# Performance work log

Hardware: AMD Instinct MI355X
Metric: run time of the kernel (lower is better)

Reference implementation:

```python
import jax, jax.numpy as jnp
import numpy as np

B, S, D = 4, 4096, 64   # batch, seq_len, input_size
H, HD = 4, 16           # num_heads, head_dim


def setup_inputs() -> dict:
    key = jax.random.key(0)
    ks = jax.random.split(key, 9)
    sd = 1.0 / np.sqrt(D)          # torch Linear default uniform(-1/sqrt(fan_in), ...)
    so = 1.0 / np.sqrt(H * HD)
    u = lambda k, shape, s: jax.random.uniform(k, shape, jnp.float32, -s, s)
    return {
        "x": jax.random.normal(ks[0], (B, S, D), jnp.float32),
        "Wq": u(ks[1], (H, D, HD), sd), "bq": u(ks[2], (H, HD), sd),
        "Wk": u(ks[3], (H, D, HD), sd), "bk": u(ks[4], (H, HD), sd),
        "Wv": u(ks[5], (H, D, HD), sd), "bv": u(ks[6], (H, HD), sd),
        "Wo": u(ks[7], (H * HD, D), so), "bo": u(ks[8], (D,), so),
    }


def reference(x, Wq, bq, Wk, bk, Wv, bv, Wo, bo):
    # Batched per-head projections (fuses the original per-head Linear loop)
    q = jnp.einsum('bsd,hde->bhse', x, Wq) + bq[None, :, None, :]
    k = jnp.einsum('bsd,hde->bhse', x, Wk) + bk[None, :, None, :]
    v = jnp.einsum('bsd,hde->bhse', x, Wv) + bv[None, :, None, :]
    # scores: [B, H, S(query), S(key)]
    scores = jnp.einsum('bhse,bhte->bhst', q, k) / np.sqrt(HD).astype(np.float32)
    # FAITHFUL quirk: torch Softmax(dim=1) on [B,S,S] normalizes over the QUERY axis
    w = jax.nn.softmax(scores, axis=2)
    attended = jnp.einsum('bhst,bhte->bhse', w, v)          # [B,H,S,HD]
    concat = attended.transpose(0, 2, 1, 3).reshape(B, S, H * HD)
    out = concat @ Wo + bo                                   # [B,S,D]
    # FAITHFUL quirk: final softmax over the sequence axis (dim=1)
    return jax.nn.softmax(out, axis=1)
```

## Files before the change

### kernel.cpp

```cpp
#include <hip/hip_runtime.h>
#include <hip/hip_bf16.h>


#define BB 4
#define SS 4096
#define DD 64
#define HH 4
#define HDD 16

typedef unsigned int u32;
typedef unsigned short u16;
typedef __attribute__((ext_vector_type(8))) short bfrag;
typedef __attribute__((ext_vector_type(4))) float floatx4;
typedef __attribute__((ext_vector_type(16))) float floatx16;
typedef __attribute__((ext_vector_type(2))) u32 u32x2;
typedef __attribute__((ext_vector_type(4))) u32 u32x4;

#define LOG2E 1.4426950408889634074f
#define QSCALE (LOG2E * 0.25f)

__device__ __forceinline__ float fexp2(float x) {
#if __has_builtin(__builtin_amdgcn_exp2f)
  return __builtin_amdgcn_exp2f(x);
#else
  float r; asm("v_exp_f32 %0, %1" : "=v"(r) : "v"(x)); return r;
#endif
}
__device__ __forceinline__ float frcp(float x) {
#if __has_builtin(__builtin_amdgcn_rcpf)
  return __builtin_amdgcn_rcpf(x);
#else
  float r; asm("v_rcp_f32 %0, %1" : "=v"(r) : "v"(x)); return r;
#endif
}

__device__ __forceinline__ u16 f2bf(float f) {
  u32 u = __builtin_bit_cast(u32, f);
  return (u16)((u + 0x7FFFu + ((u >> 16) & 1u)) >> 16);
}
__device__ __forceinline__ u32 pack_bf(float lo, float hi) {
#if __has_builtin(__builtin_amdgcn_perm)
  return __builtin_amdgcn_perm(__builtin_bit_cast(u32, hi),
                               __builtin_bit_cast(u32, lo), 0x07060302u);
#else
  u32 a = __builtin_bit_cast(u32, lo);
  u32 b = __builtin_bit_cast(u32, hi);
  return (a >> 16) | (b & 0xFFFF0000u);
#endif
}

__global__ __launch_bounds__(256) void k_proj(
    const float* __restrict__ x,
    const float* __restrict__ Wq, const float* __restrict__ bq,
    const float* __restrict__ Wk, const float* __restrict__ bk,
    const float* __restrict__ Wv, const float* __restrict__ bv,
    u16* __restrict__ qb, u16* __restrict__ kb, float* __restrict__ vf)
{
  __shared__ float xs[16 * 64];
  const int tid = threadIdx.x;
  const int blk = blockIdx.x;
  const int b   = blk >> 8;
  const int s0  = (blk & 255) << 4;
  ((float4*)xs)[tid] = ((const float4*)(x + ((size_t)b * SS + s0) * DD))[tid];
  __syncthreads();

  const int col = tid & 63, h = col >> 4, e = col & 15;
  const int rg  = tid >> 6;
  float aq[4] = {0,0,0,0}, ak[4] = {0,0,0,0}, av[4] = {0,0,0,0};
  const int wofs = h * (DD * HDD) + e;
#pragma unroll 4
  for (int d = 0; d < DD; ++d) {
    float wq = Wq[wofs + d * HDD];
    float wk = Wk[wofs + d * HDD];
    float wv = Wv[wofs + d * HDD];
    const float* xr = xs + (rg * 4) * 64 + d;
#pragma unroll
    for (int r = 0; r < 4; ++r) {
      float xv = xr[r * 64];
      aq[r] += xv * wq; ak[r] += xv * wk; av[r] += xv * wv;
    }
  }
  const float bqv = bq[col], bkv = bk[col], bvv = bv[col];
  size_t base = ((size_t)(b * HH + h) * SS + (s0 + rg * 4)) * HDD + e;
#pragma unroll
  for (int r = 0; r < 4; ++r) {
    qb[base + r * HDD] = f2bf((aq[r] + bqv) * QSCALE);
    kb[base + r * HDD] = f2bf(ak[r] + bkv);
    vf[base + r * HDD] = av[r] + bvv;
  }
}

__global__ __launch_bounds__(256, 8) void k_colsum(
    const u16* __restrict__ qb, const u16* __restrict__ kb,
    float* __restrict__ csp)
{
  const int tid = threadIdx.x;
  const int lane = tid & 63, w = tid >> 6;
  const int l31 = lane & 31, hl = lane >> 5;
  const int bh = blockIdx.z, chunk = blockIdx.y;
  const int t0 = blockIdx.x * 128 + w * 32;
  const size_t base = (size_t)bh * (SS * HDD);

  const bfrag kf = *(const bfrag*)(kb + base + (size_t)(t0 + l31) * HDD + hl * 8);
  const u16* qp = qb + base + (size_t)l31 * HDD + hl * 8;
  const floatx16 z16 = {0.f};
  float c = 0.f;
  const int s0 = chunk * 1024;
#pragma unroll 2
  for (int s = s0; s < s0 + 1024; s += 32) {
    bfrag qfr = *(const bfrag*)(qp + (size_t)s * HDD);
    floatx16 d = __builtin_amdgcn_mfma_f32_32x32x16_bf16(qfr, kf, z16, 0, 0, 0);
#pragma unroll
    for (int i = 0; i < 16; ++i) c += fexp2(d[i]);
  }
  c += __shfl_xor(c, 32, 64);
  if (hl == 0)
    csp[((size_t)bh * 4 + chunk) * SS + t0 + l31] = c;
}

__global__ __launch_bounds__(256, 6) void k_attn(
    const u16* __restrict__ qb, const u16* __restrict__ kb,
    const float* __restrict__ vf, const float* __restrict__ csp,
    float* __restrict__ attp)
{
  __shared__ __align__(16) u16 vls[16 * 520];
  __shared__ float rcs[512];
  const int tid  = threadIdx.x;
  const int lane = tid & 63, w = tid >> 6;
  const int l31 = lane & 31, hl = lane >> 5;
  const int bh = blockIdx.z, b = bh >> 2, h = bh & 3;
  const int tq = blockIdx.y;
  const int s0 = blockIdx.x * 128 + w * 32;
  const size_t base = (size_t)bh * (SS * HDD);

  const bfrag qf = *(const bfrag*)(qb + base + (size_t)(s0 + l31) * HDD + hl * 8);
  const u16* kp = kb + base + (size_t)l31 * HDD + hl * 8;
  const u16* vrow = vls + (l31 & 15) * 520 + hl * 16;
  const floatx16 z16 = {0.f};
  floatx16 acc = {0.f};

  for (int th = 0; th < 2; ++th) {
    const int tb = tq * 1024 + th * 512;
    __syncthreads();
    {
      const float* cp0 = csp + (size_t)bh * 4 * SS + tb;
#pragma unroll
      for (int i = 0; i < 2; ++i) {
        int j = i * 256 + tid;
        rcs[j] = frcp(cp0[j] + cp0[j + SS] + cp0[j + 2 * SS] + cp0[j + 3 * SS]);
      }
    }
    __syncthreads();
    {
      const float4* vsrc = (const float4*)(vf + base + (size_t)tb * HDD);
#pragma unroll
      for (int kk = 0; kk < 8; ++kk) {
        int c = kk * 256 + tid;
        int tl = c >> 2, g = c & 3;
        float4 vv = vsrc[c];
        float rc = rcs[tl];
        int i5 = tl >> 5, t5 = tl & 31;
        int sub = ((t5 >> 2) & 1) * 16 + ((t5 >> 3) << 2) + (t5 & 3);
        u16* wp = vls + i5 * 32 + sub;
        wp[(4 * g + 0) * 520] = f2bf(vv.x * rc);
        wp[(4 * g + 1) * 520] = f2bf(vv.y * rc);
        wp[(4 * g + 2) * 520] = f2bf(vv.z * rc);
        wp[(4 * g + 3) * 520] = f2bf(vv.w * rc);
      }
    }
    __syncthreads();

#pragma unroll 2
    for (int it = 0; it < 16; ++it) {
      bfrag kf = *(const bfrag*)(kp + (size_t)(tb + it * 32) * HDD);
      floatx16 d = __builtin_amdgcn_mfma_f32_32x32x16_bf16(kf, qf, z16, 0, 0, 0);
      u32 wr[8];
#pragma unroll
      for (int p = 0; p < 8; ++p)
        wr[p] = pack_bf(fexp2(d[2 * p]), fexp2(d[2 * p + 1]));
      const u16* va = vrow + it * 32;
      u32x4 af0 = *(const u32x4*)(va);
      u32x4 af1 = *(const u32x4*)(va + 8);
      u32x4 ef0 = {wr[0], wr[1], wr[2], wr[3]};
      u32x4 ef1 = {wr[4], wr[5], wr[6], wr[7]};
      acc = __builtin_amdgcn_mfma_f32_32x32x16_bf16(
          __builtin_bit_cast(bfrag, af0), __builtin_bit_cast(bfrag, ef0), acc, 0, 0, 0);
      acc = __builtin_amdgcn_mfma_f32_32x32x16_bf16(
          __builtin_bit_cast(bfrag, af1), __builtin_bit_cast(bfrag, ef1), acc, 0, 0, 0);
    }
  }

  float* ao = attp + (((size_t)tq * BB + b) * SS + s0 + l31) * (HH * HDD)
            + h * HDD + 4 * hl;
  float4 lo4 = {acc[0], acc[1], acc[2], acc[3]};
  float4 hi4 = {acc[4], acc[5], acc[6], acc[7]};
  *(float4*)ao       = lo4;
  *(float4*)(ao + 8) = hi4;
}

__global__ __launch_bounds__(256) void k_oproj(
    const float* __restrict__ att, const float* __restrict__ Wo,
    const float* __restrict__ bo, float* __restrict__ outp,
    float* __restrict__ part)
{
  __shared__ float wols[64 * 64];
  __shared__ float red[4][64];
  const int tid = threadIdx.x;
  const int blk = blockIdx.x;
  const int b = blk >> 9, s0 = (blk & 511) << 3;
#pragma unroll
  for (int i = 0; i < 4; ++i)
    ((float4*)wols)[tid + 256 * i] = ((const float4*)Wo)[tid + 256 * i];
  __syncthreads();

  const int d = tid & 63, sg = tid >> 6;
  const float bov = bo[d];
  const size_t so = (size_t)BB * SS * 16;
  float es = 0.f;
#pragma unroll
  for (int r = 0; r < 2; ++r) {
    int s = s0 + sg * 2 + r;
    const floatx4* row = (const floatx4*)(att + ((size_t)b * SS + s) * 64);
    float acc = bov;
#pragma unroll
    for (int j = 0; j < 16; ++j) {
      floatx4 c = (row[j] + row[j + so]) + (row[j + 2 * so] + row[j + 3 * so]);
      acc += c[0] * wols[(4*j+0)*64 + d] + c[1] * wols[(4*j+1)*64 + d]
           + c[2] * wols[(4*j+2)*64 + d] + c[3] * wols[(4*j+3)*64 + d];
    }
    outp[((size_t)b * SS + s) * 64 + d] = acc;
    es += fexp2(acc * LOG2E);
  }
  red[sg][d] = es;
  __syncthreads();
  if (tid < 64)
    part[((size_t)b * 512 + (blk & 511)) * 64 + tid] =
        red[0][tid] + red[1][tid] + red[2][tid] + red[3][tid];
}

__global__ __launch_bounds__(256) void k_softmax(
    const float* __restrict__ outp, const float* __restrict__ part,
    float* __restrict__ out)
{
  __shared__ float red[4][64];
  __shared__ float rs[64];
  const int tid = threadIdx.x, d = tid & 63, sg = tid >> 6;
  const int st = blockIdx.x;
  const int b = blockIdx.y;
  {
    float e = 0.f;
    const float* pp = part + ((size_t)b * 512 + sg * 128) * 64 + d;
#pragma unroll 8
    for (int c = 0; c < 128; ++c) e += pp[c * 64];
    red[sg][d] = e;
  }
  __syncthreads();
  if (tid < 64)
    rs[tid] = frcp(red[0][tid] + red[1][tid] + red[2][tid] + red[3][tid]);
  __syncthreads();
  const float r = rs[d];
  const size_t rowbase = ((size_t)b * SS + st * 64 + sg * 16) * 64 + d;
#pragma unroll 4
  for (int i = 0; i < 16; ++i)
    out[rowbase + i * 64] = fexp2(outp[rowbase + i * 64] * LOG2E) * r;
}

extern "C" void kernel_launch(void* const* d_in, const int* in_sizes, int n_in,
                              void* d_out, int out_size, void* d_ws, size_t ws_size,
                              hipStream_t stream) {
  const float* x  = (const float*)d_in[0];
  const float* Wq = (const float*)d_in[1];
  const float* bq = (const float*)d_in[2];
  const float* Wk = (const float*)d_in[3];
  const float* bk = (const float*)d_in[4];
  const float* Wv = (const float*)d_in[5];
  const float* bv = (const float*)d_in[6];
  const float* Wo = (const float*)d_in[7];
  const float* bo = (const float*)d_in[8];

  char* ws = (char*)d_ws;
  constexpr size_t QB_OFF  = 0;
  constexpr size_t KB_OFF  = (size_t)2  << 20;
  constexpr size_t VF_OFF  = (size_t)4  << 20;
  constexpr size_t CSP_OFF = (size_t)10 << 20;
  constexpr size_t ATT_OFF = (size_t)11 << 20;
  constexpr size_t OUT_OFF = (size_t)27 << 20;
  constexpr size_t PT_OFF  = (size_t)31 << 20;

  u16*   qb   = (u16*)  (ws + QB_OFF);
  u16*   kb   = (u16*)  (ws + KB_OFF);
  float* vf   = (float*)(ws + VF_OFF);
  float* csp  = (float*)(ws + CSP_OFF);
  float* attp = (float*)(ws + ATT_OFF);
  float* outp = (float*)(ws + OUT_OFF);
  float* part = (float*)(ws + PT_OFF);
  float* out  = (float*)d_out;

  hipLaunchKernelGGL(k_proj,    dim3(1024),       dim3(256), 0, stream,
                     x, Wq, bq, Wk, bk, Wv, bv, qb, kb, vf);
  hipLaunchKernelGGL(k_colsum,  dim3(32, 4, 16),  dim3(256), 0, stream, qb, kb, csp);
  hipLaunchKernelGGL(k_attn,    dim3(32, 4, 16),  dim3(256), 0, stream,
                     qb, kb, vf, csp, attp);
  hipLaunchKernelGGL(k_oproj,   dim3(2048),       dim3(256), 0, stream,
                     attp, Wo, bo, outp, part);
  hipLaunchKernelGGL(k_softmax, dim3(64, 4),      dim3(256), 0, stream, outp, part, out);
}
```

Before: 206.6 us.

## Double-buffer V tiles in LDS with register prefetch in attention kernel

The attention kernel now loads all 1024 reciprocal column sums once and splits the key range into four 256-wide chunks. V is double-buffered in LDS: the next chunk's V is fetched into registers before the MFMA loop and scaled into the other buffer afterward, so global loads overlap compute and fewer barriers are needed. The smaller LDS footprint allows raising the occupancy hint from 6 to 7 blocks, at the cost of extra registers for the prefetched float4s.

After: 210.8 us. 1.02x slower.

```diff
diff --git a/kernel.cpp b/kernel.cpp
--- a/kernel.cpp
+++ b/kernel.cpp
@@ -118,13 +118,13 @@
     csp[((size_t)bh * 4 + chunk) * SS + t0 + l31] = c;
 }
 
-__global__ __launch_bounds__(256, 6) void k_attn(
+__global__ __launch_bounds__(256, 7) void k_attn(
     const u16* __restrict__ qb, const u16* __restrict__ kb,
     const float* __restrict__ vf, const float* __restrict__ csp,
     float* __restrict__ attp)
 {
-  __shared__ __align__(16) u16 vls[16 * 520];
-  __shared__ float rcs[512];
+  __shared__ __align__(16) u16 vls[2][16][264];
+  __shared__ float rcs[1024];
   const int tid  = threadIdx.x;
   const int lane = tid & 63, w = tid >> 6;
   const int l31 = lane & 31, hl = lane >> 5;
@@ -132,46 +132,56 @@
   const int tq = blockIdx.y;
   const int s0 = blockIdx.x * 128 + w * 32;
   const size_t base = (size_t)bh * (SS * HDD);
+  const int tbq = tq * 1024;
+
+  {
+    const float* cp0 = csp + (size_t)bh * 4 * SS + tbq;
+#pragma unroll
+    for (int i = 0; i < 4; ++i) {
+      int j = i * 256 + tid;
+      rcs[j] = frcp(cp0[j] + cp0[j + SS] + cp0[j + 2 * SS] + cp0[j + 3 * SS]);
+    }
+  }
+  __syncthreads();
 
   const bfrag qf = *(const bfrag*)(qb + base + (size_t)(s0 + l31) * HDD + hl * 8);
   const u16* kp = kb + base + (size_t)l31 * HDD + hl * 8;
-  const u16* vrow = vls + (l31 & 15) * 520 + hl * 16;
   const floatx16 z16 = {0.f};
   floatx16 acc = {0.f};
 
-  for (int th = 0; th < 2; ++th) {
-    const int tb = tq * 1024 + th * 512;
-    __syncthreads();
-    {
-      const float* cp0 = csp + (size_t)bh * 4 * SS + tb;
-#pragma unroll
-      for (int i = 0; i < 2; ++i) {
-        int j = i * 256 + tid;
-        rcs[j] = frcp(cp0[j] + cp0[j + SS] + cp0[j + 2 * SS] + cp0[j + 3 * SS]);
-      }
-    }
-    __syncthreads();
-    {
-      const float4* vsrc = (const float4*)(vf + base + (size_t)tb * HDD);
-#pragma unroll
-      for (int kk = 0; kk < 8; ++kk) {
-        int c = kk * 256 + tid;
-        int tl = c >> 2, g = c & 3;
-        float4 vv = vsrc[c];
-        float rc = rcs[tl];
-        int i5 = tl >> 5, t5 = tl & 31;
-        int sub = ((t5 >> 2) & 1) * 16 + ((t5 >> 3) << 2) + (t5 & 3);
-        u16* wp = vls + i5 * 32 + sub;
-        wp[(4 * g + 0) * 520] = f2bf(vv.x * rc);
-        wp[(4 * g + 1) * 520] = f2bf(vv.y * rc);
-        wp[(4 * g + 2) * 520] = f2bf(vv.z * rc);
-        wp[(4 * g + 3) * 520] = f2bf(vv.w * rc);
-      }
-    }
-    __syncthreads();
-
+  const float4* vsrc = (const float4*)(vf + base + (size_t)tbq * HDD);
+
+  {
+#pragma unroll
+    for (int kk = 0; kk < 4; ++kk) {
+      int c = kk * 256 + tid;
+      int tl = c >> 2, g = c & 3;
+      float4 vv = vsrc[c];
+      float rc = rcs[tl];
+      int i5 = tl >> 5, t5 = tl & 31;
+      int sub = ((t5 >> 2) & 1) * 16 + ((t5 >> 3) << 2) + (t5 & 3);
+      u16* wp = &vls[0][0][0] + i5 * 32 + sub;
+      wp[(4 * g + 0) * 264] = f2bf(vv.x * rc);
+      wp[(4 * g + 1) * 264] = f2bf(vv.y * rc);
+      wp[(4 * g + 2) * 264] = f2bf(vv.z * rc);
+      wp[(4 * g + 3) * 264] = f2bf(vv.w * rc);
+    }
+  }
+  __syncthreads();
+
+#pragma unroll
+  for (int ch = 0; ch < 4; ++ch) {
+    float4 pv[4];
+    if (ch < 3) {
+#pragma unroll
+      for (int kk = 0; kk < 4; ++kk)
+        pv[kk] = vsrc[(ch + 1) * 1024 + kk * 256 + tid];
+    }
+
+    const u16* vrow = &vls[ch & 1][0][0] + (l31 & 15) * 264 + hl * 16;
+    const int tb = tbq + ch * 256;
 #pragma unroll 2
-    for (int it = 0; it < 16; ++it) {
+    for (int it = 0; it < 8; ++it) {
       bfrag kf = *(const bfrag*)(kp + (size_t)(tb + it * 32) * HDD);
       floatx16 d = __builtin_amdgcn_mfma_f32_32x32x16_bf16(kf, qf, z16, 0, 0, 0);
       u32 wr[8];
@@ -188,6 +198,24 @@
       acc = __builtin_amdgcn_mfma_f32_32x32x16_bf16(
           __builtin_bit_cast(bfrag, af1), __builtin_bit_cast(bfrag, ef1), acc, 0, 0, 0);
     }
+
+    if (ch < 3) {
+      u16* dstb = &vls[(ch + 1) & 1][0][0];
+#pragma unroll
+      for (int kk = 0; kk < 4; ++kk) {
+        int c = kk * 256 + tid;
+        int tl = c >> 2, g = c & 3;
+        float rc = rcs[(ch + 1) * 256 + tl];
+        int i5 = tl >> 5, t5 = tl & 31;
+        int sub = ((t5 >> 2) & 1) * 16 + ((t5 >> 3) << 2) + (t5 & 3);
+        u16* wp = dstb + i5 * 32 + sub;
+        wp[(4 * g + 0) * 264] = f2bf(pv[kk].x * rc);
+        wp[(4 * g + 1) * 264] = f2bf(pv[kk].y * rc);
+        wp[(4 * g + 2) * 264] = f2bf(pv[kk].z * rc);
+        wp[(4 * g + 3) * 264] = f2bf(pv[kk].w * rc);
+      }
+    }
+    __syncthreads();
   }
 
   float* ao = attp + (((size_t)tq * BB + b) * SS + s0 + l31) * (HH * HDD)
```

## Shrink attention LDS staging to 256-key chunks and split colsum accumulators

Applied to the files above, without the earlier changes.

The attention kernel now stages V in four 256-key chunks instead of two 512-key halves. This halves the LDS tile and drops the shared reciprocal array by computing each column-sum reciprocal inline. The launch bound is raised to 8 blocks per CU to allow higher occupancy. The colsum kernel splits its exp2 accumulation into four independent partial sums to shorten the dependent add chain. In exchange there are more barriers, and the four column-sum loads are repeated per thread.

New measurement: 209.3 us. About the same (+1.3%).

```diff
diff --git a/kernel.cpp b/kernel.cpp
--- a/kernel.cpp
+++ b/kernel.cpp
@@ -104,27 +104,32 @@
   const bfrag kf = *(const bfrag*)(kb + base + (size_t)(t0 + l31) * HDD + hl * 8);
   const u16* qp = qb + base + (size_t)l31 * HDD + hl * 8;
   const floatx16 z16 = {0.f};
-  float c = 0.f;
+  float c0 = 0.f, c1 = 0.f, c2 = 0.f, c3 = 0.f;
   const int s0 = chunk * 1024;
 #pragma unroll 2
   for (int s = s0; s < s0 + 1024; s += 32) {
     bfrag qfr = *(const bfrag*)(qp + (size_t)s * HDD);
     floatx16 d = __builtin_amdgcn_mfma_f32_32x32x16_bf16(qfr, kf, z16, 0, 0, 0);
 #pragma unroll
-    for (int i = 0; i < 16; ++i) c += fexp2(d[i]);
-  }
+    for (int i = 0; i < 4; ++i) {
+      c0 += fexp2(d[4 * i + 0]);
+      c1 += fexp2(d[4 * i + 1]);
+      c2 += fexp2(d[4 * i + 2]);
+      c3 += fexp2(d[4 * i + 3]);
+    }
+  }
+  float c = (c0 + c1) + (c2 + c3);
   c += __shfl_xor(c, 32, 64);
   if (hl == 0)
     csp[((size_t)bh * 4 + chunk) * SS + t0 + l31] = c;
 }
 
-__global__ __launch_bounds__(256, 6) void k_attn(
+__global__ __launch_bounds__(256, 8) void k_attn(
     const u16* __restrict__ qb, const u16* __restrict__ kb,
     const float* __restrict__ vf, const float* __restrict__ csp,
     float* __restrict__ attp)
 {
-  __shared__ __align__(16) u16 vls[16 * 520];
-  __shared__ float rcs[512];
+  __shared__ __align__(16) u16 vls[16][264];
   const int tid  = threadIdx.x;
   const int lane = tid & 63, w = tid >> 6;
   const int l31 = lane & 31, hl = lane >> 5;
@@ -132,46 +137,40 @@
   const int tq = blockIdx.y;
   const int s0 = blockIdx.x * 128 + w * 32;
   const size_t base = (size_t)bh * (SS * HDD);
+  const int tbq = tq * 1024;
 
   const bfrag qf = *(const bfrag*)(qb + base + (size_t)(s0 + l31) * HDD + hl * 8);
   const u16* kp = kb + base + (size_t)l31 * HDD + hl * 8;
-  const u16* vrow = vls + (l31 & 15) * 520 + hl * 16;
   const floatx16 z16 = {0.f};
   floatx16 acc = {0.f};
 
-  for (int th = 0; th < 2; ++th) {
-    const int tb = tq * 1024 + th * 512;
+  const float4* vsrc = (const float4*)(vf + base + (size_t)tbq * HDD);
+  const float* cspb = csp + (size_t)bh * 4 * SS + tbq;
+
+#pragma unroll
+  for (int ch = 0; ch < 4; ++ch) {
     __syncthreads();
-    {
-      const float* cp0 = csp + (size_t)bh * 4 * SS + tb;
-#pragma unroll
-      for (int i = 0; i < 2; ++i) {
-        int j = i * 256 + tid;
-        rcs[j] = frcp(cp0[j] + cp0[j + SS] + cp0[j + 2 * SS] + cp0[j + 3 * SS]);
-      }
+#pragma unroll
+    for (int kk = 0; kk < 4; ++kk) {
+      int c = kk * 256 + tid;
+      int tl = c >> 2, g = c & 3;
+      float4 vv = vsrc[ch * 1024 + c];
+      const float* cp = cspb + ch * 256 + tl;
+      float rc = frcp(cp[0] + cp[SS] + cp[2 * SS] + cp[3 * SS]);
+      int i5 = tl >> 5, t5 = tl & 31;
+      int sub = ((t5 >> 2) & 1) * 16 + ((t5 >> 3) << 2) + (t5 & 3);
+      u16* wp = &vls[0][0] + i5 * 32 + sub;
+      wp[(4 * g + 0) * 264] = f2bf(vv.x * rc);
+      wp[(4 * g + 1) * 264] = f2bf(vv.y * rc);
+      wp[(4 * g + 2) * 264] = f2bf(vv.z * rc);
+      wp[(4 * g + 3) * 264] = f2bf(vv.w * rc);
     }
     __syncthreads();
-    {
-      const float4* vsrc = (const float4*)(vf + base + (size_t)tb * HDD);
-#pragma unroll
-      for (int kk = 0; kk < 8; ++kk) {
-        int c = kk * 256 + tid;
-        int tl = c >> 2, g = c & 3;
-        float4 vv = vsrc[c];
-        float rc = rcs[tl];
-        int i5 = tl >> 5, t5 = tl & 31;
-        int sub = ((t5 >> 2) & 1) * 16 + ((t5 >> 3) << 2) + (t5 & 3);
-        u16* wp = vls + i5 * 32 + sub;
-        wp[(4 * g + 0) * 520] = f2bf(vv.x * rc);
-        wp[(4 * g + 1) * 520] = f2bf(vv.y * rc);
-        wp[(4 * g + 2) * 520] = f2bf(vv.z * rc);
-        wp[(4 * g + 3) * 520] = f2bf(vv.w * rc);
-      }
-    }
-    __syncthreads();
-
+
+    const u16* vrow = &vls[0][0] + (l31 & 15) * 264 + hl * 16;
+    const int tb = tbq + ch * 256;
 #pragma unroll 2
-    for (int it = 0; it < 16; ++it) {
+    for (int it = 0; it < 8; ++it) {
       bfrag kf = *(const bfrag*)(kp + (size_t)(tb + it * 32) * HDD);
       floatx16 d = __builtin_amdgcn_mfma_f32_32x32x16_bf16(kf, qf, z16, 0, 0, 0);
       u32 wr[8];
```
